# Optimization experiments

Measured on AMD Instinct MI355X. Metric: run time of the kernel, lower is better.

## Reference

```python
import jax, jax.numpy as jnp
from jax import lax
import numpy as np

B = 512      # instances
C = 64       # cases (segments)
HID = 1024
ATT = 128


def _conv(x, w, b):
    # torch Conv2d(kernel=5, padding=2), NCHW / OIHW layout
    y = lax.conv_general_dilated(x, w, (1, 1), [(2, 2), (2, 2)],
                                 dimension_numbers=('NCHW', 'OIHW', 'NCHW'))
    return y + b[None, :, None, None]


def _pool(x):
    # MaxPool2d(2)
    return lax.reduce_window(x, -jnp.inf, lax.max, (1, 1, 2, 2), (1, 1, 2, 2), 'VALID')


def setup_inputs() -> dict:
    key = jax.random.key(0)
    ks = jax.random.split(key, 20)

    def rn(k, shape, scale=0.05):
        return jax.random.normal(k, shape, dtype=jnp.float32) * scale

    inp = {
        'data': jax.random.normal(ks[0], (B, 3, 128, 128), dtype=jnp.float32),
        'case_ids': jnp.sort(jax.random.randint(ks[1], (B,), 0, C, dtype=jnp.int32)),
    }
    chans = [(3, 8), (8, 16), (16, 32), (32, 64), (64, 128)]
    for i, (ci, co) in enumerate(chans):
        inp[f'conv_w{i + 1}'] = rn(ks[2 + 2 * i], (co, ci, 5, 5))
        inp[f'conv_b{i + 1}'] = jnp.zeros((co,), jnp.float32)
    inp['fc_w'] = rn(ks[12], (HID, 128 * 4 * 4), 0.02)
    inp['fc_b'] = jnp.zeros((HID,), jnp.float32)
    inp['att_w1'] = rn(ks[13], (ATT, HID), 0.02)
    inp['att_b1'] = jnp.zeros((ATT,), jnp.float32)
    inp['att_w2'] = rn(ks[14], (1, ATT), 0.02)
    inp['att_b2'] = jnp.zeros((1,), jnp.float32)
    inp['clf_w'] = rn(ks[15], (1, HID), 0.02)
    inp['clf_b'] = jnp.zeros((1,), jnp.float32)
    return inp


def reference(data, case_ids, conv_w1, conv_b1, conv_w2, conv_b2, conv_w3, conv_b3,
              conv_w4, conv_b4, conv_w5, conv_b5, fc_w, fc_b,
              att_w1, att_b1, att_w2, att_b2, clf_w, clf_b):
    x = data
    for w, b in ((conv_w1, conv_b1), (conv_w2, conv_b2), (conv_w3, conv_b3),
                 (conv_w4, conv_b4), (conv_w5, conv_b5)):
        x = jax.nn.relu(_pool(_conv(x, w, b)))
    emb = x.reshape(x.shape[0], -1) @ fc_w.T + fc_b          # (B, HID)

    # --- segment (per-case) attention pooling, vectorized over all cases ---
    logits = (jnp.tanh(emb @ att_w1.T + att_b1) @ att_w2.T + att_b2)[:, 0]  # (B,)
    seg_max = jax.ops.segment_max(logits, case_ids, num_segments=C)
    seg_max = jnp.where(jnp.isfinite(seg_max), seg_max, 0.0)  # guard empty segments
    e = jnp.exp(logits - lax.stop_gradient(seg_max)[case_ids])
    denom = jax.ops.segment_sum(e, case_ids, num_segments=C)
    wgt = e / denom[case_ids]                                  # segment softmax
    aggr = jax.ops.segment_sum(wgt[:, None] * emb, case_ids, num_segments=C)  # (C, HID)

    # --- classifier ---
    return jax.nn.sigmoid(aggr @ clf_w.T + clf_b)              # (C, 1)
```

## Files before the change

kernel.cpp:

```cpp
#include <hip/hip_runtime.h>
#include <hip/hip_bf16.h>
#include <math.h>

#define BATCH 512
#define NSEG  64
#define HID   1024
#define ATT   128

typedef __attribute__((ext_vector_type(8))) __bf16 bf16x8;
typedef __attribute__((ext_vector_type(4))) __bf16 bf16x4;
typedef __attribute__((ext_vector_type(4))) float  f32x4;

typedef __attribute__((address_space(1))) const unsigned char ga_t;
typedef __attribute__((address_space(3))) unsigned char la_t;

__device__ inline void wcv(const float* __restrict__ w, __bf16* __restrict__ wt,
                           int t, int Ci, int Co) {
    int j  = t & 7;
    int t2 = t >> 3;
    int co = t2 % Co;
    int k8 = t2 / Co;
    int k  = k8 * 8 + j;
    int tap = k / Ci, ci = k % Ci;
    wt[t] = (__bf16)w[(co * Ci + ci) * 25 + tap];
}

__global__ void wprep_k(const float* __restrict__ cw1, const float* __restrict__ cw2,
                        const float* __restrict__ cw3, const float* __restrict__ cw4,
                        const float* __restrict__ cw5, const float* __restrict__ fcw,
                        __bf16* __restrict__ wt1, __bf16* __restrict__ wt2,
                        __bf16* __restrict__ wt3, __bf16* __restrict__ wt4,
                        __bf16* __restrict__ wt5, __bf16* __restrict__ wfc) {
    int t = blockIdx.x * 256 + threadIdx.x;
    if (t < 2048) {
        int j = t & 7, m = (t >> 3) & 15, k8 = t >> 7;
        int k = k8 * 8 + j, tap = k >> 2, ci = k & 3;
        float v = 0.f;
        if (m < 8 && ci < 3 && tap < 25) v = cw1[(m * 3 + ci) * 25 + tap];
        wt1[t] = (__bf16)v;
        return;
    }
    t -= 2048;
    if (t < 3200)  { wcv(cw2, wt2, t, 8, 16);   return; }
    t -= 3200;
    if (t < 12800) { wcv(cw3, wt3, t, 16, 32);  return; }
    t -= 12800;
    if (t < 51200) { wcv(cw4, wt4, t, 32, 64);  return; }
    t -= 51200;
    if (t < 204800){ wcv(cw5, wt5, t, 64, 128); return; }
    t -= 204800;
    if (t < 2097152) {
        int j = t & 7, t2 = t >> 3, o = t2 & 1023, k8 = t2 >> 10;
        wfc[t] = (__bf16)fcw[(size_t)o * 2048 + k8 * 8 + j];
    }
}

__global__ void watt_k(const float* __restrict__ w, __bf16* __restrict__ wt) {
    int t = blockIdx.x * 256 + threadIdx.x;
    if (t >= 131072) return;
    int j  = t & 7;
    int t2 = t >> 3;
    int o  = t2 & 127;
    int k8 = t2 >> 7;
    wt[t] = (__bf16)w[(size_t)o * 1024 + k8 * 8 + j];
}

__global__ __launch_bounds__(256) void conv1_mfma_k(
    const float* __restrict__ in, const __bf16* __restrict__ Wt,
    const float* __restrict__ bias, __bf16* __restrict__ out) {
    constexpr int W  = 128;
    constexpr int R  = 4;
    constexpr int RP = R + 4;
    constexpr int WP = W + 4;
    constexpr int CSTR = R * W + 4;

    __shared__ __align__(16) __bf16 xs[RP * WP * 4];
    __shared__ float cs[8 * CSTR];

    const int tid = threadIdx.x;
    const int b   = blockIdx.x >> 5;
    const int y0  = (blockIdx.x & 31) * R;
    const float* inb = in + (size_t)b * 3 * 16384;

    if (tid < RP * 4) {
        int r = tid >> 2, s = tid & 3;
        int c = (s < 2) ? s : (128 + s);
        *(bf16x4*)(xs + (r * WP + c) * 4) = (bf16x4){};
    }
    {
        int r  = tid >> 5;
        int g  = tid & 31;
        int gy = y0 + r - 2;
        int c0 = g * 4;
        bf16x8 lo = {}, hi = {};
        if ((unsigned)gy < 128u) {
            const float* p = inb + (size_t)gy * 128 + c0;
            float4 a = *(const float4*)(p);
            float4 q = *(const float4*)(p + 16384);
            float4 c = *(const float4*)(p + 32768);
            lo[0] = (__bf16)a.x; lo[1] = (__bf16)q.x; lo[2] = (__bf16)c.x;
            lo[4] = (__bf16)a.y; lo[5] = (__bf16)q.y; lo[6] = (__bf16)c.y;
            hi[0] = (__bf16)a.z; hi[1] = (__bf16)q.z; hi[2] = (__bf16)c.z;
            hi[4] = (__bf16)a.w; hi[5] = (__bf16)q.w; hi[6] = (__bf16)c.w;
        }
        *(bf16x8*)(xs + (r * WP + c0 + 2) * 4)     = lo;
        *(bf16x8*)(xs + (r * WP + c0 + 2) * 4 + 8) = hi;
    }
    __syncthreads();

    const int lane = tid & 63, wave = tid >> 6;
    const int quad = lane >> 4, l15 = lane & 15;
    constexpr int F = 8;

    int pbase[F];
    f32x4 acc[F];
#pragma unroll
    for (int f = 0; f < F; ++f) {
        pbase[f] = ((wave + 2) * WP + f * 16 + l15 + 2) * 8;
        acc[f] = f32x4{0.f, 0.f, 0.f, 0.f};
    }
    const char* xsb = (const char*)xs;

#pragma unroll
    for (int kt = 0; kt < 4; ++kt) {
        int k8 = kt * 4 + quad;
        int tap0 = k8 * 2, tap1 = tap0 + 1;
        int t0 = tap0 < 25 ? tap0 : 0;
        int t1 = tap1 < 25 ? tap1 : 0;
        int s0 = ((t0 / 5 - 2) * WP + (t0 % 5 - 2)) * 8;
        int s1 = ((t1 / 5 - 2) * WP + (t1 % 5 - 2)) * 8;
        bf16x8 av = *(const bf16x8*)(Wt + ((size_t)k8 * 16 + l15) * 8);
#pragma unroll
        for (int f = 0; f < F; ++f) {
            bf16x4 b0 = *(const bf16x4*)(xsb + pbase[f] + s0);
            bf16x4 b1 = *(const bf16x4*)(xsb + pbase[f] + s1);
            bf16x8 bv = __builtin_shufflevector(b0, b1, 0, 1, 2, 3, 4, 5, 6, 7);
            acc[f] = __builtin_amdgcn_mfma_f32_16x16x32_bf16(av, bv, acc[f], 0, 0, 0);
        }
    }

#pragma unroll
    for (int f = 0; f < F; ++f) {
        int pl = wave * 128 + f * 16 + l15;
#pragma unroll
        for (int r = 0; r < 4; ++r) {
            int m = quad * 4 + r;
            if (m < 8) cs[m * CSTR + pl] = acc[f][r];
        }
    }
    __syncthreads();

    {
        int oi  = tid >> 1;
        int cog = (tid & 1) * 4;
        int oy  = oi >> 6, ox = oi & 63;
        int pl0 = oy * 2 * 128 + ox * 2;
        float4 b4 = *(const float4*)(bias + cog);
        bf16x4 ov;
#pragma unroll
        for (int i = 0; i < 4; ++i) {
            int cr = cog + i;
            float v0 = cs[cr * CSTR + pl0],       v1 = cs[cr * CSTR + pl0 + 1];
            float v2 = cs[cr * CSTR + pl0 + 128], v3 = cs[cr * CSTR + pl0 + 129];
            float m = fmaxf(fmaxf(v0, v1), fmaxf(v2, v3)) + ((const float*)&b4)[i];
            ov[i] = (__bf16)fmaxf(m, 0.f);
        }
        size_t ob = ((size_t)b * 4096 + (size_t)(y0 / 2 + oy) * 64 + ox) * 8 + cog;
        *(bf16x4*)(out + ob) = ov;
    }
}

template<int Ci, int Co, int H, int RB, int IMGS, int OUTMODE, int CS>
__global__ __launch_bounds__(256) void conv2d_mfma_k(
    const __bf16* __restrict__ X, const __bf16* __restrict__ Wt,
    const float* __restrict__ bias, void* __restrict__ outp) {
    constexpr int W    = H;
    constexpr int PW   = W + 4;
    constexpr int PR   = RB + 4;
    constexpr int PIX  = RB * W;
    constexpr int P    = IMGS * PIX;
    constexpr int SE   = Ci + (Ci >= 16 ? 8 : 0);
    constexpr int SB   = SE * 2;
    constexpr int K    = 25 * Ci;
    constexpr int KTF  = K / 32;
    constexpr int KT   = KTF + (K % 32 != 0 ? 1 : 0);
    constexpr int NK8  = KT * 4;
    constexpr int FW   = P / 64;
    constexpr int NCOT = Co / 16 / CS;
    constexpr int C8   = Ci / 8;
    constexpr int BPI  = H / RB;
    constexpr int OW   = W / 2;

    __shared__ __align__(16) char smem[IMGS * PR * PW * SB];
    __shared__ int shtab[NK8];

    const int tid = threadIdx.x;
    const int b0  = (blockIdx.x / BPI) * IMGS;
    const int y0  = (blockIdx.x % BPI) * RB;
    const int co0 = blockIdx.y * (NCOT * 16);

    const int lane = tid & 63, wave = tid >> 6;

    if (tid < NK8) {
        int kk  = tid * 8;
        int kkc = kk < K ? kk : 0;
        int tap = kkc / Ci, cio = kkc % Ci;
        shtab[tid] = ((tap / 5 - 2) * PW + (tap % 5 - 2)) * SB + cio * 2;
    }

    if constexpr (Ci == 8 && IMGS == 1) {
        __bf16* xs = (__bf16*)smem;
        if (tid < PR * 4) {
            int r = tid >> 2, s = tid & 3;
            int c = (s < 2) ? s : (W + s);
            *(bf16x8*)(xs + (r * PW + c) * 8) = (bf16x8){};
        }
        for (int pr = wave; pr < PR; pr += 4) {
            int gy = y0 + pr - 2;
            if ((unsigned)gy < (unsigned)H) {
                const __bf16* gsrc = X + ((size_t)(b0 * H + gy) * W + lane) * 8;
                __bf16* ldst = xs + (pr * PW + 2) * 8;
                __builtin_amdgcn_global_load_lds((ga_t*)gsrc, (la_t*)ldst, 16, 0, 0);
            } else {
                *(bf16x8*)(xs + (pr * PW + 2 + lane) * 8) = (bf16x8){};
            }
        }
    } else {
        constexpr int NSLOT = IMGS * PR * PW * C8;
        for (int i = tid; i < NSLOT; i += 256) {
            int s   = i % C8;
            int t2  = i / C8;
            int pc  = t2 % PW;
            int t3  = t2 / PW;
            int pr  = t3 % PR;
            int img = t3 / PR;
            int gy  = y0 + pr - 2;
            int gx  = pc - 2;
            bf16x8 v = {};
            if ((unsigned)gy < (unsigned)H && (unsigned)gx < (unsigned)W)
                v = *(const bf16x8*)(X + (((size_t)(b0 + img) * H + gy) * W + gx) * Ci + s * 8);
            *(bf16x8*)(smem + ((size_t)(img * PR + pr) * PW + pc) * SB + s * 16) = v;
        }
    }
    __syncthreads();

    const int quad = lane >> 4, l15 = lane & 15;

    int pbase[FW];
    f32x4 acc[FW][NCOT];
    int rg = 0, ch = 0, gbase = 0, img5 = 0;
    if constexpr (W >= 16) {
        constexpr int C16 = W / 16;
        ch = wave % C16;
        rg = wave / C16;
#pragma unroll
        for (int f = 0; f < FW; ++f) {
            int row = rg * FW + f;
            pbase[f] = ((row + 2) * PW + ch * 16 + l15 + 2) * SB;
        }
    } else {
        img5  = wave >> 1;
        gbase = (wave & 1) * FW;
#pragma unroll
        for (int f = 0; f < FW; ++f) {
            int g    = gbase + f;
            int row0 = 2 * g + (l15 >> 3);
            pbase[f] = ((img5 * PR + row0 + 2) * PW + (l15 & 7) + 2) * SB;
        }
    }
#pragma unroll
    for (int f = 0; f < FW; ++f)
#pragma unroll
        for (int c = 0; c < NCOT; ++c) acc[f][c] = f32x4{0.f, 0.f, 0.f, 0.f};

    const bf16x8 BZ = {};

    bf16x8 avc[NCOT];
    {
        int k8 = quad;
#pragma unroll
        for (int c = 0; c < NCOT; ++c)
            avc[c] = *(const bf16x8*)(Wt + ((size_t)k8 * Co + co0 + c * 16 + l15) * 8);
    }
#pragma unroll 2
    for (int kt = 0; kt < KT; ++kt) {
        bf16x8 avn[NCOT];
        {
            int k8n = (kt + 1) * 4 + quad;
            if (kt + 1 >= KT || k8n * 8 >= K) k8n = 0;
#pragma unroll
            for (int c = 0; c < NCOT; ++c)
                avn[c] = *(const bf16x8*)(Wt + ((size_t)k8n * Co + co0 + c * 16 + l15) * 8);
        }
        int k8 = kt * 4 + quad;
        bool kok = true;
        if (K % 32 != 0 && kt == KT - 1) {
            kok = k8 * 8 < K;
            if (!kok) k8 = 0;
        }
        int shift = shtab[k8];
        bf16x8 bv[FW];
#pragma unroll
        for (int f = 0; f < FW; ++f) {
            bv[f] = *(const bf16x8*)(smem + pbase[f] + shift);
            if (!kok) bv[f] = BZ;
        }
#pragma unroll
        for (int c = 0; c < NCOT; ++c)
#pragma unroll
            for (int f = 0; f < FW; ++f)
                acc[f][c] = __builtin_amdgcn_mfma_f32_16x16x32_bf16(avc[c], bv[f], acc[f][c], 0, 0, 0);
#pragma unroll
        for (int c = 0; c < NCOT; ++c) avc[c] = avn[c];
    }

    if constexpr (W >= 16) {
#pragma unroll
        for (int fp = 0; fp < FW / 2; ++fp) {
            int f0  = 2 * fp;
            int row = rg * FW + f0;
            int oy  = (y0 + row) >> 1;
            int ox  = (ch * 16 + l15) >> 1;
            bool on = (l15 & 1) == 0;
#pragma unroll
            for (int c = 0; c < NCOT; ++c) {
                float4 bb = *(const float4*)(bias + co0 + c * 16 + quad * 4);
                bf16x4 ov;
#pragma unroll
                for (int r = 0; r < 4; ++r) {
                    float v0 = acc[f0][c][r];
                    float h0 = fmaxf(v0, __shfl_xor(v0, 1));
                    float v1 = acc[f0 + 1][c][r];
                    float h1 = fmaxf(v1, __shfl_xor(v1, 1));
                    float m  = fmaxf(h0, h1) + ((const float*)&bb)[r];
                    ov[r] = (__bf16)fmaxf(m, 0.f);
                }
                if (on)
                    *(bf16x4*)((__bf16*)outp +
                        (((size_t)b0 * (H / 2) + oy) * OW + ox) * Co + co0 + c * 16 + quad * 4) = ov;
            }
        }
    } else {
#pragma unroll
        for (int f = 0; f < FW; ++f) {
            int g   = gbase + f;
            bool on = ((l15 & 1) == 0) && (l15 < 8);
            int ox  = (l15 & 7) >> 1;
#pragma unroll
            for (int c = 0; c < NCOT; ++c) {
                float4 bb = *(const float4*)(bias + co0 + c * 16 + quad * 4);
#pragma unroll
                for (int r = 0; r < 4; ++r) {
                    float v  = acc[f][c][r];
                    float h  = fmaxf(v, __shfl_xor(v, 1));
                    float m2 = fmaxf(h, __shfl_xor(h, 8));
                    float m  = fmaxf(m2 + ((const float*)&bb)[r], 0.f);
                    if (on)
                        ((__bf16*)outp)[(size_t)(b0 + img5) * 2048 +
                            (co0 + c * 16 + quad * 4 + r) * 16 + g * 4 + ox] = (__bf16)m;
                }
            }
        }
    }
}

__global__ __launch_bounds__(256) void fc_mfma_k(
    const __bf16* __restrict__ Xb, const __bf16* __restrict__ Wfc,
    const float* __restrict__ bias, float* __restrict__ emb,
    __bf16* __restrict__ embb) {
    const int tid  = threadIdx.x;
    const int lane = tid & 63, wave = tid >> 6;
    const int quad = lane >> 4, l15 = lane & 15;
    const int n    = blockIdx.x * 64 + wave * 16 + l15;
    const int co0  = blockIdx.y * 16;

    f32x4 acc = f32x4{0.f, 0.f, 0.f, 0.f};

#pragma unroll 8
    for (int kt = 0; kt < 64; ++kt) {
        int k8 = kt * 4 + quad;
        bf16x8 av = *(const bf16x8*)(Wfc + ((size_t)k8 * 1024 + co0 + l15) * 8);
        bf16x8 bv = *(const bf16x8*)(Xb + (size_t)n * 2048 + k8 * 8);
        acc = __builtin_amdgcn_mfma_f32_16x16x32_bf16(av, bv, acc, 0, 0, 0);
    }

    float4 b4 = *(const float4*)(bias + co0 + quad * 4);
    f32x4 v = acc;
    v[0] += b4.x; v[1] += b4.y; v[2] += b4.z; v[3] += b4.w;
    *(f32x4*)(emb + (size_t)n * 1024 + co0 + quad * 4) = v;
    bf16x4 eb;
    eb[0] = (__bf16)v[0]; eb[1] = (__bf16)v[1];
    eb[2] = (__bf16)v[2]; eb[3] = (__bf16)v[3];
    *(bf16x4*)(embb + (size_t)n * 1024 + co0 + quad * 4) = eb;
}

__global__ __launch_bounds__(256) void att_mfma_k(
    const __bf16* __restrict__ embb, const __bf16* __restrict__ Wa,
    const float* __restrict__ b1, const float* __restrict__ w2,
    const float* __restrict__ b2, float* __restrict__ logits) {
    const int tid = threadIdx.x, lane = tid & 63, wave = tid >> 6;
    const int quad = lane >> 4, l15 = lane & 15;
    const int n = blockIdx.x * 16 + l15;

    f32x4 acc[2];
    acc[0] = f32x4{0.f, 0.f, 0.f, 0.f};
    acc[1] = f32x4{0.f, 0.f, 0.f, 0.f};

#pragma unroll 4
    for (int kt = 0; kt < 32; ++kt) {
        int k8 = kt * 4 + quad;
        bf16x8 bv = *(const bf16x8*)(embb + (size_t)n * 1024 + k8 * 8);
#pragma unroll
        for (int t = 0; t < 2; ++t) {
            int o0 = (wave * 2 + t) * 16;
            bf16x8 av = *(const bf16x8*)(Wa + ((size_t)k8 * 128 + o0 + l15) * 8);
            acc[t] = __builtin_amdgcn_mfma_f32_16x16x32_bf16(av, bv, acc[t], 0, 0, 0);
        }
    }

    float s = 0.f;
#pragma unroll
    for (int t = 0; t < 2; ++t) {
#pragma unroll
        for (int r = 0; r < 4; ++r) {
            int o = (wave * 2 + t) * 16 + quad * 4 + r;
            s += tanhf(acc[t][r] + b1[o]) * w2[o];
        }
    }
    s += __shfl_xor(s, 16);
    s += __shfl_xor(s, 32);

    __shared__ float part[4][16];
    if (lane < 16) part[wave][l15] = s;
    __syncthreads();
    if (tid < 16)
        logits[blockIdx.x * 16 + tid] =
            part[0][tid] + part[1][tid] + part[2][tid] + part[3][tid] + b2[0];
}

__global__ __launch_bounds__(256) void segment_k(
    const float* __restrict__ emb, const float* __restrict__ logits,
    const int* __restrict__ cid, const float* __restrict__ clf_w,
    const float* __restrict__ clf_b, float* __restrict__ out) {
    const int c = blockIdx.x;
    const int t = threadIdx.x;
    __shared__ int cids[BATCH];
    __shared__ float red[256];
    for (int i = t; i < BATCH; i += 256) cids[i] = cid[i];
    __syncthreads();

    int lo, hi;
    {
        int l = 0, r = BATCH;
        while (l < r) { int m = (l + r) >> 1; if (cids[m] < c) l = m + 1; else r = m; }
        lo = l;
        r = BATCH;
        while (l < r) { int m = (l + r) >> 1; if (cids[m] <= c) l = m + 1; else r = m; }
        hi = l;
    }

    float lm = -1e30f;
    for (int b = lo + t; b < hi; b += 256) lm = fmaxf(lm, logits[b]);
    red[t] = lm; __syncthreads();
    for (int s = 128; s > 0; s >>= 1) {
        if (t < s) red[t] = fmaxf(red[t], red[t + s]);
        __syncthreads();
    }
    float smax = red[0]; __syncthreads();

    float ls = 0.f;
    for (int b = lo + t; b < hi; b += 256) ls += expf(logits[b] - smax);
    red[t] = ls; __syncthreads();
    for (int s = 128; s > 0; s >>= 1) {
        if (t < s) red[t] += red[t + s];
        __syncthreads();
    }
    float denom = red[0]; __syncthreads();
    float inv = (denom > 0.f) ? 1.f / denom : 0.f;

    const int h0 = t * 4;
    float g0 = 0.f, g1 = 0.f, g2 = 0.f, g3 = 0.f;
    for (int b = lo; b < hi; ++b) {
        float wgt = expf(logits[b] - smax) * inv;
        float4 ev = *(const float4*)(emb + (size_t)b * HID + h0);
        g0 = fmaf(wgt, ev.x, g0);
        g1 = fmaf(wgt, ev.y, g1);
        g2 = fmaf(wgt, ev.z, g2);
        g3 = fmaf(wgt, ev.w, g3);
    }
    float4 cw = *(const float4*)(clf_w + h0);
    float ca = g0 * cw.x + g1 * cw.y + g2 * cw.z + g3 * cw.w;
    red[t] = ca; __syncthreads();
    for (int s = 128; s > 0; s >>= 1) {
        if (t < s) red[t] += red[t + s];
        __syncthreads();
    }
    if (t == 0) out[c] = 1.f / (1.f + expf(-(red[0] + clf_b[0])));
}

extern "C" void kernel_launch(void* const* d_in, const int* in_sizes, int n_in,
                              void* d_out, int out_size, void* d_ws, size_t ws_size,
                              hipStream_t stream) {
    const float* data = (const float*)d_in[0];
    const int*   cid  = (const int*)d_in[1];
    const float* cw1 = (const float*)d_in[2],  * cb1 = (const float*)d_in[3];
    const float* cw2 = (const float*)d_in[4],  * cb2 = (const float*)d_in[5];
    const float* cw3 = (const float*)d_in[6],  * cb3 = (const float*)d_in[7];
    const float* cw4 = (const float*)d_in[8],  * cb4 = (const float*)d_in[9];
    const float* cw5 = (const float*)d_in[10], * cb5 = (const float*)d_in[11];
    const float* fcw = (const float*)d_in[12], * fcb = (const float*)d_in[13];
    const float* aw1 = (const float*)d_in[14], * ab1 = (const float*)d_in[15];
    const float* aw2 = (const float*)d_in[16], * ab2 = (const float*)d_in[17];
    const float* clw = (const float*)d_in[18], * clb = (const float*)d_in[19];
    float* out = (float*)d_out;

    char* wsb = (char*)d_ws;
    __bf16* x1  = (__bf16*)(wsb);
    __bf16* x2  = (__bf16*)(wsb + 33554432);
    __bf16* x3  = (__bf16*)(wsb + 50331648);
    __bf16* x4  = (__bf16*)(wsb + 58720256);
    __bf16* x5b = (__bf16*)(wsb + 62914560);
    float*  emb = (float*) (wsb + 65011712);
    float*  lg  = (float*) (wsb + 67108864);
    __bf16* wt2 = (__bf16*)(wsb + 67110912);
    __bf16* wt3 = (__bf16*)(wsb + 67117312);
    __bf16* wt4 = (__bf16*)(wsb + 67142912);
    __bf16* wt5 = (__bf16*)(wsb + 67245312);
    __bf16* wfc = (__bf16*)(wsb + 67654912);
    __bf16* wt1 = (__bf16*)(wsb + 71849216);
    __bf16* wa   = (__bf16*)(wsb);
    __bf16* embb = (__bf16*)(wsb + 1048576);

    wprep_k<<<9263, 256, 0, stream>>>(cw1, cw2, cw3, cw4, cw5, fcw,
                                      wt1, wt2, wt3, wt4, wt5, wfc);

    conv1_mfma_k<<<16384, 256, 0, stream>>>(data, wt1, cb1, x1);

    conv2d_mfma_k<8,  16,  64, 8, 1, 0, 1><<<4096, 256, 0, stream>>>(x1, wt2, cb2, x2);
    watt_k<<<512, 256, 0, stream>>>(aw1, wa);
    conv2d_mfma_k<16, 32,  32, 8, 1, 0, 1><<<2048, 256, 0, stream>>>(x2, wt3, cb3, x3);
    conv2d_mfma_k<32, 64,  16, 8, 1, 0, 2><<<dim3(1024, 2), 256, 0, stream>>>(x3, wt4, cb4, x4);
    conv2d_mfma_k<64, 128, 8,  8, 2, 1, 4><<<dim3(256, 4), 256, 0, stream>>>(x4, wt5, cb5, x5b);

    fc_mfma_k<<<dim3(8, 64), 256, 0, stream>>>(x5b, wfc, fcb, emb, embb);
    att_mfma_k<<<32, 256, 0, stream>>>(embb, wa, ab1, aw2, ab2, lg);
    segment_k<<<NSEG, 256, 0, stream>>>(emb, lg, cid, clw, clb, out);
}
```

Baseline: 351.7 us.

## Restructure conv staging loop, prefetch shift table, fully unroll short K, k8-major FC input

Result: no change. 350.0 us (median of 2 runs) (-0.5%).

```diff
diff --git a/kernel.cpp b/kernel.cpp
--- a/kernel.cpp
+++ b/kernel.cpp
@@ -188,6 +188,7 @@
     constexpr int FW   = P / 64;
     constexpr int NCOT = Co / 16 / CS;
     constexpr int C8   = Ci / 8;
+    constexpr int LC8  = (C8 == 1 ? 0 : (C8 == 2 ? 1 : (C8 == 4 ? 2 : 3)));
     constexpr int BPI  = H / RB;
     constexpr int OW   = W / 2;
 
@@ -226,20 +227,21 @@
             }
         }
     } else {
-        constexpr int NSLOT = IMGS * PR * PW * C8;
-        for (int i = tid; i < NSLOT; i += 256) {
-            int s   = i % C8;
-            int t2  = i / C8;
-            int pc  = t2 % PW;
-            int t3  = t2 / PW;
-            int pr  = t3 % PR;
-            int img = t3 / PR;
+        for (int rr = wave; rr < IMGS * PR; rr += 4) {
+            int img = (IMGS == 1) ? 0 : (rr / PR);
+            int pr  = rr - img * PR;
             int gy  = y0 + pr - 2;
-            int gx  = pc - 2;
-            bf16x8 v = {};
-            if ((unsigned)gy < (unsigned)H && (unsigned)gx < (unsigned)W)
-                v = *(const bf16x8*)(X + (((size_t)(b0 + img) * H + gy) * W + gx) * Ci + s * 8);
-            *(bf16x8*)(smem + ((size_t)(img * PR + pr) * PW + pc) * SB + s * 16) = v;
+            char* rowp = smem + ((size_t)(img * PR + pr) * PW) * SB;
+            const __bf16* grow = X + (((size_t)(b0 + img) * H + gy) * W) * Ci;
+            for (int j = lane; j < PW * C8; j += 64) {
+                int pc = j >> LC8;
+                int s  = j & (C8 - 1);
+                int gx = pc - 2;
+                bf16x8 v = {};
+                if ((unsigned)gy < (unsigned)H && (unsigned)gx < (unsigned)W)
+                    v = *(const bf16x8*)(grow + (size_t)gx * Ci + s * 8);
+                *(bf16x8*)(rowp + (size_t)pc * SB + s * 16) = v;
+            }
         }
     }
     __syncthreads();
@@ -276,33 +278,33 @@
     const bf16x8 BZ = {};
 
     bf16x8 avc[NCOT];
+    int shc;
     {
         int k8 = quad;
+        shc = shtab[k8];
 #pragma unroll
         for (int c = 0; c < NCOT; ++c)
             avc[c] = *(const bf16x8*)(Wt + ((size_t)k8 * Co + co0 + c * 16 + l15) * 8);
     }
-#pragma unroll 2
-    for (int kt = 0; kt < KT; ++kt) {
+
+    auto body = [&](int kt) {
         bf16x8 avn[NCOT];
+        int shn;
         {
             int k8n = (kt + 1) * 4 + quad;
             if (kt + 1 >= KT || k8n * 8 >= K) k8n = 0;
+            shn = shtab[k8n];
 #pragma unroll
             for (int c = 0; c < NCOT; ++c)
                 avn[c] = *(const bf16x8*)(Wt + ((size_t)k8n * Co + co0 + c * 16 + l15) * 8);
         }
-        int k8 = kt * 4 + quad;
         bool kok = true;
-        if (K % 32 != 0 && kt == KT - 1) {
-            kok = k8 * 8 < K;
-            if (!kok) k8 = 0;
-        }
-        int shift = shtab[k8];
+        if (K % 32 != 0 && kt == KT - 1)
+            kok = (kt * 4 + quad) * 8 < K;
         bf16x8 bv[FW];
 #pragma unroll
         for (int f = 0; f < FW; ++f) {
-            bv[f] = *(const bf16x8*)(smem + pbase[f] + shift);
+            bv[f] = *(const bf16x8*)(smem + pbase[f] + shc);
             if (!kok) bv[f] = BZ;
         }
 #pragma unroll
@@ -310,8 +312,17 @@
 #pragma unroll
             for (int f = 0; f < FW; ++f)
                 acc[f][c] = __builtin_amdgcn_mfma_f32_16x16x32_bf16(avc[c], bv[f], acc[f][c], 0, 0, 0);
+        shc = shn;
 #pragma unroll
         for (int c = 0; c < NCOT; ++c) avc[c] = avn[c];
+    };
+
+    if constexpr (KT <= 16) {
+#pragma unroll
+        for (int kt = 0; kt < KT; ++kt) body(kt);
+    } else {
+#pragma unroll 2
+        for (int kt = 0; kt < KT; ++kt) body(kt);
     }
 
     if constexpr (W >= 16) {
@@ -355,9 +366,15 @@
                     float h  = fmaxf(v, __shfl_xor(v, 1));
                     float m2 = fmaxf(h, __shfl_xor(h, 8));
                     float m  = fmaxf(m2 + ((const float*)&bb)[r], 0.f);
-                    if (on)
-                        ((__bf16*)outp)[(size_t)(b0 + img5) * 2048 +
-                            (co0 + c * 16 + quad * 4 + r) * 16 + g * 4 + ox] = (__bf16)m;
+                    if (on) {
+                        if (OUTMODE == 1) {
+                            int k = (co0 + c * 16 + quad * 4 + r) * 16 + g * 4 + ox;
+                            ((__bf16*)outp)[((size_t)(k >> 3) * BATCH + (b0 + img5)) * 8 + (k & 7)] = (__bf16)m;
+                        } else {
+                            ((__bf16*)outp)[(size_t)(b0 + img5) * 2048 +
+                                (co0 + c * 16 + quad * 4 + r) * 16 + g * 4 + ox] = (__bf16)m;
+                        }
+                    }
                 }
             }
         }
@@ -380,7 +397,7 @@
     for (int kt = 0; kt < 64; ++kt) {
         int k8 = kt * 4 + quad;
         bf16x8 av = *(const bf16x8*)(Wfc + ((size_t)k8 * 1024 + co0 + l15) * 8);
-        bf16x8 bv = *(const bf16x8*)(Xb + (size_t)n * 2048 + k8 * 8);
+        bf16x8 bv = *(const bf16x8*)(Xb + ((size_t)k8 * BATCH + n) * 8);
         acc = __builtin_amdgcn_mfma_f32_16x16x32_bf16(av, bv, acc, 0, 0, 0);
     }
 
```
